# Performance work log

Hardware: AMD Instinct MI355X
Metric: run time of the kernel (lower is better)

The kernel has to match this reference:

```python
import jax, jax.numpy as jnp
import numpy as np

GLM_HIDDEN = 256
POS_EMB_DIM = 64
LN_EPS = 1e-5


def _pair_indices(seq_len, K):
    # emo index i (row), cau index j (col); keep |j-i| <= K (static mask)
    i = np.repeat(np.arange(seq_len), seq_len)
    j = np.tile(np.arange(seq_len), seq_len)
    rel = j - i
    keep = np.abs(rel) <= K
    return i[keep], j[keep], rel[keep]


def setup_inputs() -> dict:
    key = jax.random.key(0)
    ks = jax.random.split(key, 8)
    B, S, D, P, K = 32, 128, GLM_HIDDEN, POS_EMB_DIM, 8
    doc_sents_h = jax.random.normal(ks[0], (B, S, D), dtype=jnp.float32)
    pos_emb = jax.random.normal(ks[1], (2 * K + 1, P), dtype=jnp.float32) * 0.1
    in_dim = 2 * D + P
    W1 = jax.random.normal(ks[2], (D, in_dim), dtype=jnp.float32) * (1.0 / np.sqrt(in_dim))
    b1 = jnp.zeros((D,), dtype=jnp.float32)
    ln_g = jnp.ones((D,), dtype=jnp.float32)
    ln_b = jnp.zeros((D,), dtype=jnp.float32)
    W2 = jax.random.normal(ks[3], (1, D), dtype=jnp.float32) * (1.0 / np.sqrt(D))
    b2 = jnp.zeros((1,), dtype=jnp.float32)
    return {"doc_sents_h": doc_sents_h, "pos_emb": pos_emb, "W1": W1, "b1": b1,
            "ln_g": ln_g, "ln_b": ln_b, "W2": W2, "b2": b2, "K": K}


def reference(doc_sents_h, pos_emb, W1, b1, ln_g, ln_b, W2, b2, K):
    B, S, D = doc_sents_h.shape
    ii, jj, rel = _pair_indices(S, K)          # static numpy, shape [n_couple]
    # couples = [H_i ; H_j] for in-window pairs (replaces broadcast-concat + masked_select)
    couples = jnp.concatenate([doc_sents_h[:, ii], doc_sents_h[:, jj]], axis=-1)  # [B,n,2D]
    rel_idx = jnp.asarray(rel + K, dtype=jnp.int32)
    rpe = pos_emb[rel_idx]                     # [n, P]
    rf = jnp.asarray(rel, dtype=jnp.float32)
    kernel = jnp.exp(-jnp.square(rf[:, None] - rf[None, :]))  # [n, n]
    rpe = kernel @ rpe                         # [n, P] (same for every batch elem)
    pair = jnp.concatenate(
        [couples, jnp.broadcast_to(rpe[None], (B,) + rpe.shape)], axis=-1)  # [B,n,2D+P]
    h = jnp.einsum('bnf,df->bnd', pair, W1) + b1
    mu = jnp.mean(h, axis=-1, keepdims=True)
    var = jnp.mean(jnp.square(h - mu), axis=-1, keepdims=True)
    h = (h - mu) * jax.lax.rsqrt(var + LN_EPS) * ln_g + ln_b
    h = jax.nn.elu(h)                          # dropout is identity in eval
    scores = (jnp.einsum('bnd,od->bno', h, W2) + b2)[..., 0]  # [B, n]
    emo_cau_pos = jnp.stack([jnp.asarray(ii + 1), jnp.asarray(jj + 1)], axis=1)  # [n, 2]
    return scores, emo_cau_pos
```

## Files before the change

kernel.cpp:

```cpp
#include <hip/hip_runtime.h>
#include <math.h>

constexpr int kB = 32;
constexpr int kS = 128;
constexpr int kD = 256;
constexpr int kK = 8;
constexpr int kNPair = 2104;
constexpr int kInDim = 2 * kD + 64;
constexpr int kRows = kB * kS;

typedef __attribute__((ext_vector_type(8))) short short8;
typedef __attribute__((ext_vector_type(4))) float f32x4;

__device__ inline ushort f2b(float f) {
  union { float f; uint u; } v; v.f = f;
  uint r = v.u + 0x7FFF + ((v.u >> 16) & 1);
  return (ushort)(r >> 16);
}

__global__ __launch_bounds__(256) void gemm_uv_r(
    const float* __restrict__ H, const float* __restrict__ W1,
    const float* __restrict__ pos_emb, const float* __restrict__ b1,
    float* __restrict__ U, float* __restrict__ V, float* __restrict__ R) {
  __shared__ ushort As[64 * 256];
  __shared__ ushort Bs[64 * 256];
  const int tid = threadIdx.x;

  if (blockIdx.x == 512) {
    float* pe = (float*)As;
    for (int idx = tid; idx < 17 * 64; idx += 256) pe[idx] = pos_emb[idx];
    __syncthreads();
    const int d = tid;
    float w[64];
    const float* wr = W1 + d * kInDim + 2 * kD;
#pragma unroll
    for (int q = 0; q < 16; ++q) {
      float4 t4 = *(const float4*)(wr + q * 4);
      w[q * 4 + 0] = t4.x; w[q * 4 + 1] = t4.y;
      w[q * 4 + 2] = t4.z; w[q * 4 + 3] = t4.w;
    }
    float acc[17];
#pragma unroll
    for (int t = 0; t < 17; ++t) acc[t] = 0.f;
    for (int u = 0; u < 17; ++u) {
      float m = 0.f;
#pragma unroll
      for (int p = 0; p < 64; ++p) m += pe[u * 64 + p] * w[p];
      int au = u - kK; if (au < 0) au = -au;
      m *= (float)(kS - au);
#pragma unroll
      for (int t = 0; t < 17; ++t) {
        int dd = t - u;
        acc[t] += expf((float)(-(dd * dd))) * m;
      }
    }
#pragma unroll
    for (int t = 0; t < 17; ++t) R[t * kD + d] = acc[t] + b1[d];
    return;
  }

  const int mt = blockIdx.x & 63;
  const int nt = blockIdx.x >> 6;
  const int m0 = mt * 64;
  const int side = (nt >= 4) ? kD : 0;
  const int wbase = (nt & 3) * 64;

#pragma unroll
  for (int l = 0; l < 16; ++l) {
    int c = tid + l * 256;
    int row = c >> 6;
    int kq = (c & 63) << 2;
    int sw = (row << 8) + (kq ^ ((row & 7) << 3));
    float4 a4 = *(const float4*)(H + (m0 + row) * kD + kq);
    ushort4 au; au.x = f2b(a4.x); au.y = f2b(a4.y); au.z = f2b(a4.z); au.w = f2b(a4.w);
    *(ushort4*)(As + sw) = au;
    float4 b4 = *(const float4*)(W1 + (wbase + row) * kInDim + side + kq);
    ushort4 bu; bu.x = f2b(b4.x); bu.y = f2b(b4.y); bu.z = f2b(b4.z); bu.w = f2b(b4.w);
    *(ushort4*)(Bs + sw) = bu;
  }
  __syncthreads();

  const int lane = tid & 63;
  const int w = tid >> 6;
  const int wm = (w & 1) * 32;
  const int wn = (w >> 1) * 32;
  const int lr = lane & 15;
  const int lk = (lane >> 4) * 8;

  f32x4 acc[2][2] = {{{0.f,0.f,0.f,0.f},{0.f,0.f,0.f,0.f}},
                     {{0.f,0.f,0.f,0.f},{0.f,0.f,0.f,0.f}}};
#pragma unroll
  for (int kk = 0; kk < 8; ++kk) {
    const int k0 = kk * 32 + lk;
    short8 a[2], b[2];
#pragma unroll
    for (int mf = 0; mf < 2; ++mf) {
      int ra = wm + mf * 16 + lr;
      a[mf] = *(const short8*)(const void*)(As + (ra << 8) + (k0 ^ ((ra & 7) << 3)));
      int rb = wn + mf * 16 + lr;
      b[mf] = *(const short8*)(const void*)(Bs + (rb << 8) + (k0 ^ ((rb & 7) << 3)));
    }
#pragma unroll
    for (int mf = 0; mf < 2; ++mf)
#pragma unroll
      for (int nf = 0; nf < 2; ++nf)
        acc[mf][nf] = __builtin_amdgcn_mfma_f32_16x16x32_bf16(a[mf], b[nf], acc[mf][nf], 0, 0, 0);
  }

  const int rowg0 = m0 + wm + (lane >> 4) * 4;
  const int colg0 = nt * 64 + wn + lr;
#pragma unroll
  for (int mf = 0; mf < 2; ++mf)
#pragma unroll
    for (int nf = 0; nf < 2; ++nf) {
      int colg = colg0 + nf * 16;
      float* dst = (colg < kD) ? (U + colg) : (V + (colg - kD));
#pragma unroll
      for (int r = 0; r < 4; ++r) {
        int rowg = rowg0 + mf * 16 + r;
        dst[rowg * kD] = acc[mf][nf][r];
      }
    }
}

__global__ __launch_bounds__(256) void pair_score2(
    const float* __restrict__ U, const float* __restrict__ V,
    const float* __restrict__ R,
    const float* __restrict__ ln_g, const float* __restrict__ ln_b,
    const float* __restrict__ W2, const float* __restrict__ b2,
    float* __restrict__ out) {
  const int tid = threadIdx.x;
  const int l16 = tid & 15;
  const int grp = (blockIdx.x * 256 + tid) >> 4;
  const int t = grp % 17;
  const int bi = grp / 17;
  const int i = bi & (kS - 1);
  const int b = bi >> 7;
  const int j = i - kK + t;
  const bool valid = (j >= 0) && (j < kS);
  const int jc = valid ? j : 0;

  int start_i;
  if (i <= 8)        start_i = (i * i + 17 * i) / 2;
  else if (i <= 120) start_i = 100 + (i - 8) * 17;
  else { int m = i - 120; start_i = 2004 + 16 * m - (m * (m - 1)) / 2; }
  const int lower = (i - kK > 0) ? (i - kK) : 0;
  const int p = start_i + (j - lower);

  const float* Urow = U + (b * kS + i) * kD;
  const float* Vrow = V + (b * kS + jc) * kD;
  const float* Rrow = R + t * kD;

  float h[16];
  float s = 0.f, qs = 0.f;
#pragma unroll
  for (int q = 0; q < 4; ++q) {
    const int d = q * 64 + l16 * 4;
    float4 u4 = *(const float4*)(Urow + d);
    float4 v4 = *(const float4*)(Vrow + d);
    float4 r4 = *(const float4*)(Rrow + d);
    float h0 = u4.x + v4.x + r4.x;
    float h1 = u4.y + v4.y + r4.y;
    float h2 = u4.z + v4.z + r4.z;
    float h3 = u4.w + v4.w + r4.w;
    h[q * 4 + 0] = h0; h[q * 4 + 1] = h1; h[q * 4 + 2] = h2; h[q * 4 + 3] = h3;
    s += h0 + h1 + h2 + h3;
    qs += h0 * h0 + h1 * h1 + h2 * h2 + h3 * h3;
  }
#pragma unroll
  for (int off = 8; off > 0; off >>= 1) {
    s  += __shfl_xor(s, off);
    qs += __shfl_xor(qs, off);
  }
  const float mu = s * (1.0f / kD);
  const float var = qs * (1.0f / kD) - mu * mu;
  const float rs = rsqrtf(var + 1e-5f);

  float dot = 0.f;
#pragma unroll
  for (int q = 0; q < 4; ++q) {
    const int d = q * 64 + l16 * 4;
    float4 g4  = *(const float4*)(ln_g + d);
    float4 be4 = *(const float4*)(ln_b + d);
    float4 w4  = *(const float4*)(W2 + d);
    float y0 = (h[q * 4 + 0] - mu) * rs * g4.x + be4.x;
    float y1 = (h[q * 4 + 1] - mu) * rs * g4.y + be4.y;
    float y2 = (h[q * 4 + 2] - mu) * rs * g4.z + be4.z;
    float y3 = (h[q * 4 + 3] - mu) * rs * g4.w + be4.w;
    y0 = y0 > 0.f ? y0 : (__expf(y0) - 1.0f);
    y1 = y1 > 0.f ? y1 : (__expf(y1) - 1.0f);
    y2 = y2 > 0.f ? y2 : (__expf(y2) - 1.0f);
    y3 = y3 > 0.f ? y3 : (__expf(y3) - 1.0f);
    dot += y0 * w4.x + y1 * w4.y + y2 * w4.z + y3 * w4.w;
  }
#pragma unroll
  for (int off = 8; off > 0; off >>= 1) dot += __shfl_xor(dot, off);

  if (l16 == 0 && valid) {
    out[b * kNPair + p] = dot + b2[0];
    if (b == 0) {
      float* posout = out + kB * kNPair;
      posout[p * 2 + 0] = (float)(i + 1);
      posout[p * 2 + 1] = (float)(j + 1);
    }
  }
}

extern "C" void kernel_launch(void* const* d_in, const int* in_sizes, int n_in,
                              void* d_out, int out_size, void* d_ws, size_t ws_size,
                              hipStream_t stream) {
  const float* H       = (const float*)d_in[0];
  const float* pos_emb = (const float*)d_in[1];
  const float* W1      = (const float*)d_in[2];
  const float* b1      = (const float*)d_in[3];
  const float* ln_g    = (const float*)d_in[4];
  const float* ln_b    = (const float*)d_in[5];
  const float* W2      = (const float*)d_in[6];
  const float* b2      = (const float*)d_in[7];
  float* out = (float*)d_out;

  float* U = (float*)d_ws;
  float* V = U + kRows * kD;
  float* R = V + kRows * kD;

  gemm_uv_r<<<513, 256, 0, stream>>>(H, W1, pos_emb, b1, U, V, R);
  const int n_groups = kB * kS * 17;
  pair_score2<<<n_groups / 16, 256, 0, stream>>>(U, V, R, ln_g, ln_b, W2, b2, out);
}
```

Measured before the change: 42.66 us.

## Fuse projection GEMM, positional term and pair scoring into one kernel

Result: faster. 39.95 us (-6.3%).

```diff
diff --git a/kernel.cpp b/kernel.cpp
--- a/kernel.cpp
+++ b/kernel.cpp
@@ -6,8 +6,8 @@
 constexpr int kD = 256;
 constexpr int kK = 8;
 constexpr int kNPair = 2104;
-constexpr int kInDim = 2 * kD + 64;
-constexpr int kRows = kB * kS;
+constexpr int kInDim = 576;
+constexpr int kRS = 264;
 
 typedef __attribute__((ext_vector_type(8))) short short8;
 typedef __attribute__((ext_vector_type(4))) float f32x4;
@@ -18,190 +18,216 @@
   return (ushort)(r >> 16);
 }
 
-__global__ __launch_bounds__(256) void gemm_uv_r(
-    const float* __restrict__ H, const float* __restrict__ W1,
-    const float* __restrict__ pos_emb, const float* __restrict__ b1,
-    float* __restrict__ U, float* __restrict__ V, float* __restrict__ R) {
-  __shared__ ushort As[64 * 256];
-  __shared__ ushort Bs[64 * 256];
-  const int tid = threadIdx.x;
-
-  if (blockIdx.x == 512) {
-    float* pe = (float*)As;
-    for (int idx = tid; idx < 17 * 64; idx += 256) pe[idx] = pos_emb[idx];
-    __syncthreads();
-    const int d = tid;
-    float w[64];
-    const float* wr = W1 + d * kInDim + 2 * kD;
-#pragma unroll
-    for (int q = 0; q < 16; ++q) {
-      float4 t4 = *(const float4*)(wr + q * 4);
-      w[q * 4 + 0] = t4.x; w[q * 4 + 1] = t4.y;
-      w[q * 4 + 2] = t4.z; w[q * 4 + 3] = t4.w;
-    }
-    float acc[17];
-#pragma unroll
-    for (int t = 0; t < 17; ++t) acc[t] = 0.f;
-    for (int u = 0; u < 17; ++u) {
-      float m = 0.f;
-#pragma unroll
-      for (int p = 0; p < 64; ++p) m += pe[u * 64 + p] * w[p];
-      int au = u - kK; if (au < 0) au = -au;
-      m *= (float)(kS - au);
-#pragma unroll
-      for (int t = 0; t < 17; ++t) {
-        int dd = t - u;
-        acc[t] += expf((float)(-(dd * dd))) * m;
-      }
-    }
-#pragma unroll
-    for (int t = 0; t < 17; ++t) R[t * kD + d] = acc[t] + b1[d];
-    return;
-  }
-
-  const int mt = blockIdx.x & 63;
-  const int nt = blockIdx.x >> 6;
-  const int m0 = mt * 64;
-  const int side = (nt >= 4) ? kD : 0;
-  const int wbase = (nt & 3) * 64;
-
-#pragma unroll
-  for (int l = 0; l < 16; ++l) {
-    int c = tid + l * 256;
-    int row = c >> 6;
-    int kq = (c & 63) << 2;
-    int sw = (row << 8) + (kq ^ ((row & 7) << 3));
-    float4 a4 = *(const float4*)(H + (m0 + row) * kD + kq);
-    ushort4 au; au.x = f2b(a4.x); au.y = f2b(a4.y); au.z = f2b(a4.z); au.w = f2b(a4.w);
-    *(ushort4*)(As + sw) = au;
-    float4 b4 = *(const float4*)(W1 + (wbase + row) * kInDim + side + kq);
-    ushort4 bu; bu.x = f2b(b4.x); bu.y = f2b(b4.y); bu.z = f2b(b4.z); bu.w = f2b(b4.w);
-    *(ushort4*)(Bs + sw) = bu;
-  }
-  __syncthreads();
-
-  const int lane = tid & 63;
-  const int w = tid >> 6;
-  const int wm = (w & 1) * 32;
-  const int wn = (w >> 1) * 32;
-  const int lr = lane & 15;
-  const int lk = (lane >> 4) * 8;
-
-  f32x4 acc[2][2] = {{{0.f,0.f,0.f,0.f},{0.f,0.f,0.f,0.f}},
-                     {{0.f,0.f,0.f,0.f},{0.f,0.f,0.f,0.f}}};
-#pragma unroll
-  for (int kk = 0; kk < 8; ++kk) {
-    const int k0 = kk * 32 + lk;
-    short8 a[2], b[2];
-#pragma unroll
-    for (int mf = 0; mf < 2; ++mf) {
-      int ra = wm + mf * 16 + lr;
-      a[mf] = *(const short8*)(const void*)(As + (ra << 8) + (k0 ^ ((ra & 7) << 3)));
-      int rb = wn + mf * 16 + lr;
-      b[mf] = *(const short8*)(const void*)(Bs + (rb << 8) + (k0 ^ ((rb & 7) << 3)));
-    }
-#pragma unroll
-    for (int mf = 0; mf < 2; ++mf)
-#pragma unroll
-      for (int nf = 0; nf < 2; ++nf)
-        acc[mf][nf] = __builtin_amdgcn_mfma_f32_16x16x32_bf16(a[mf], b[nf], acc[mf][nf], 0, 0, 0);
-  }
-
-  const int rowg0 = m0 + wm + (lane >> 4) * 4;
-  const int colg0 = nt * 64 + wn + lr;
-#pragma unroll
-  for (int mf = 0; mf < 2; ++mf)
-#pragma unroll
-    for (int nf = 0; nf < 2; ++nf) {
-      int colg = colg0 + nf * 16;
-      float* dst = (colg < kD) ? (U + colg) : (V + (colg - kD));
-#pragma unroll
-      for (int r = 0; r < 4; ++r) {
-        int rowg = rowg0 + mf * 16 + r;
-        dst[rowg * kD] = acc[mf][nf][r];
-      }
-    }
-}
-
-__global__ __launch_bounds__(256) void pair_score2(
-    const float* __restrict__ U, const float* __restrict__ V,
-    const float* __restrict__ R,
+__global__ __launch_bounds__(256, 1) void fused_all(
+    const float* __restrict__ H, const float* __restrict__ pos_emb,
+    const float* __restrict__ W1, const float* __restrict__ b1,
     const float* __restrict__ ln_g, const float* __restrict__ ln_b,
     const float* __restrict__ W2, const float* __restrict__ b2,
     float* __restrict__ out) {
+  __shared__ __align__(16) ushort sH[48 * 256];
+  __shared__ __align__(16) ushort sW[64 * 256];
+  __shared__ __align__(16) ushort sKpe[32 * 64];
+  __shared__ float sU[16 * kRS];
+  __shared__ float sV[48 * kRS];
+  __shared__ float sR[17 * kRS];
+  __shared__ float sG[256], sBe[256], sWo[256], sB1[256];
+  __shared__ float sB2v;
+
   const int tid = threadIdx.x;
-  const int l16 = tid & 15;
-  const int grp = (blockIdx.x * 256 + tid) >> 4;
-  const int t = grp % 17;
-  const int bi = grp / 17;
-  const int i = bi & (kS - 1);
-  const int b = bi >> 7;
-  const int j = i - kK + t;
-  const bool valid = (j >= 0) && (j < kS);
-  const int jc = valid ? j : 0;
-
-  int start_i;
-  if (i <= 8)        start_i = (i * i + 17 * i) / 2;
-  else if (i <= 120) start_i = 100 + (i - 8) * 17;
-  else { int m = i - 120; start_i = 2004 + 16 * m - (m * (m - 1)) / 2; }
-  const int lower = (i - kK > 0) ? (i - kK) : 0;
-  const int p = start_i + (j - lower);
-
-  const float* Urow = U + (b * kS + i) * kD;
-  const float* Vrow = V + (b * kS + jc) * kD;
-  const float* Rrow = R + t * kD;
-
-  float h[16];
-  float s = 0.f, qs = 0.f;
+  const int b = blockIdx.x >> 3;
+  const int i0 = (blockIdx.x & 7) << 4;
+  int ws_ = i0 - 16; if (ws_ < 0) ws_ = 0; if (ws_ > 80) ws_ = 80;
+  const int ws = ws_;
+  const int oi = i0 - ws;
+
+  sG[tid] = ln_g[tid]; sBe[tid] = ln_b[tid]; sWo[tid] = W2[tid]; sB1[tid] = b1[tid];
+  if (tid == 0) sB2v = b2[0];
+
+#pragma unroll
+  for (int l = 0; l < 12; ++l) {
+    int c = tid + l * 256, row = c >> 6, kq = (c & 63) << 2;
+    float4 a4 = *(const float4*)(H + (b * kS + ws + row) * kD + kq);
+    ushort4 u; u.x = f2b(a4.x); u.y = f2b(a4.y); u.z = f2b(a4.z); u.w = f2b(a4.w);
+    *(ushort4*)&sH[row * 256 + (kq ^ ((row & 7) << 3))] = u;
+  }
+#pragma unroll
+  for (int l = 0; l < 16; ++l) {
+    int c = tid + l * 256, d = c >> 4, kq = (c & 15) << 2;
+    float4 a4 = *(const float4*)(W1 + d * kInDim + 512 + kq);
+    ushort4 u; u.x = f2b(a4.x); u.y = f2b(a4.y); u.z = f2b(a4.z); u.w = f2b(a4.w);
+    *(ushort4*)&sW[d * 64 + (kq ^ ((d & 7) << 3))] = u;
+  }
+  {
+    const int pg = (tid & 15) << 2;
+#pragma unroll
+    for (int pass = 0; pass < 2; ++pass) {
+      int t = (tid >> 4) + pass * 16;
+      float a0 = 0.f, a1 = 0.f, a2 = 0.f, a3 = 0.f;
+      if (t < 17) {
+        for (int u = 0; u < 17; ++u) {
+          int du = t - u, au = u - kK; if (au < 0) au = -au;
+          float wt = __expf((float)(-(du * du))) * (float)(kS - au);
+          float4 pe = *(const float4*)(pos_emb + u * 64 + pg);
+          a0 += wt * pe.x; a1 += wt * pe.y; a2 += wt * pe.z; a3 += wt * pe.w;
+        }
+      }
+      ushort4 u; u.x = f2b(a0); u.y = f2b(a1); u.z = f2b(a2); u.w = f2b(a3);
+      *(ushort4*)&sKpe[t * 64 + (pg ^ ((t & 7) << 3))] = u;
+    }
+  }
+  __syncthreads();
+
+  const int lane = tid & 63;
+  const int w = tid >> 6;
+  const int lr = lane & 15;
+  const int lk = (lane >> 4) << 3;
+  const int swz = (lr & 7) << 3;
+  const int r0 = (lane >> 4) << 2;
+
+  {
+    f32x4 racc[2][4] = {{{0,0,0,0},{0,0,0,0},{0,0,0,0},{0,0,0,0}},
+                        {{0,0,0,0},{0,0,0,0},{0,0,0,0},{0,0,0,0}}};
+#pragma unroll
+    for (int kk = 0; kk < 2; ++kk) {
+      int k0 = (kk << 5) + lk;
+      short8 a0 = *(const short8*)(const void*)&sKpe[lr * 64 + (k0 ^ swz)];
+      short8 a1 = *(const short8*)(const void*)&sKpe[(16 + lr) * 64 + (k0 ^ swz)];
+#pragma unroll
+      for (int n = 0; n < 4; ++n) {
+        int drow = ((w << 2) + n) * 16 + lr;
+        short8 bf = *(const short8*)(const void*)&sW[drow * 64 + (k0 ^ swz)];
+        racc[0][n] = __builtin_amdgcn_mfma_f32_16x16x32_bf16(a0, bf, racc[0][n], 0, 0, 0);
+        racc[1][n] = __builtin_amdgcn_mfma_f32_16x16x32_bf16(a1, bf, racc[1][n], 0, 0, 0);
+      }
+    }
+#pragma unroll
+    for (int m = 0; m < 2; ++m)
+#pragma unroll
+      for (int r = 0; r < 4; ++r) {
+        int t = m * 16 + r0 + r;
+        if (t < 17) {
+#pragma unroll
+          for (int n = 0; n < 4; ++n) {
+            int d = ((w << 2) + n) * 16 + lr;
+            sR[t * kRS + d] = racc[m][n][r] + sB1[d];
+          }
+        }
+      }
+  }
+  __syncthreads();
+
+  for (int nt = 0; nt < 8; ++nt) {
+#pragma unroll
+    for (int l = 0; l < 16; ++l) {
+      int c = tid + l * 256, row = c >> 6, kq = (c & 63) << 2;
+      int cg = (nt << 6) + row;
+      const float* src = W1 + (cg & 255) * kInDim + ((cg < 256) ? 0 : 256) + kq;
+      float4 a4 = *(const float4*)src;
+      ushort4 u; u.x = f2b(a4.x); u.y = f2b(a4.y); u.z = f2b(a4.z); u.w = f2b(a4.w);
+      *(ushort4*)&sW[row * 256 + (kq ^ ((row & 7) << 3))] = u;
+    }
+    __syncthreads();
+    f32x4 acc[3] = {{0,0,0,0},{0,0,0,0},{0,0,0,0}};
+    const int brow = (w << 4) + lr;
+#pragma unroll
+    for (int kk = 0; kk < 8; ++kk) {
+      int k0 = (kk << 5) + lk;
+      short8 bf = *(const short8*)(const void*)&sW[brow * 256 + (k0 ^ swz)];
+#pragma unroll
+      for (int m = 0; m < 3; ++m) {
+        short8 af = *(const short8*)(const void*)&sH[(m * 16 + lr) * 256 + (k0 ^ swz)];
+        acc[m] = __builtin_amdgcn_mfma_f32_16x16x32_bf16(af, bf, acc[m], 0, 0, 0);
+      }
+    }
+    const int cg = (nt << 6) + (w << 4) + lr;
+#pragma unroll
+    for (int m = 0; m < 3; ++m)
+#pragma unroll
+      for (int r = 0; r < 4; ++r) {
+        int rw = m * 16 + r0 + r;
+        float val = acc[m][r];
+        if (cg < 256) {
+          unsigned ur = (unsigned)(rw - oi);
+          if (ur < 16u) sU[ur * kRS + cg] = val;
+        } else {
+          sV[rw * kRS + (cg - 256)] = val;
+        }
+      }
+    __syncthreads();
+  }
+
+  const int g = tid >> 4, l16 = tid & 15;
+  float4 Gp[4], Bp[4], Wp[4];
 #pragma unroll
   for (int q = 0; q < 4; ++q) {
-    const int d = q * 64 + l16 * 4;
-    float4 u4 = *(const float4*)(Urow + d);
-    float4 v4 = *(const float4*)(Vrow + d);
-    float4 r4 = *(const float4*)(Rrow + d);
-    float h0 = u4.x + v4.x + r4.x;
-    float h1 = u4.y + v4.y + r4.y;
-    float h2 = u4.z + v4.z + r4.z;
-    float h3 = u4.w + v4.w + r4.w;
-    h[q * 4 + 0] = h0; h[q * 4 + 1] = h1; h[q * 4 + 2] = h2; h[q * 4 + 3] = h3;
-    s += h0 + h1 + h2 + h3;
-    qs += h0 * h0 + h1 * h1 + h2 * h2 + h3 * h3;
-  }
-#pragma unroll
-  for (int off = 8; off > 0; off >>= 1) {
-    s  += __shfl_xor(s, off);
-    qs += __shfl_xor(qs, off);
-  }
-  const float mu = s * (1.0f / kD);
-  const float var = qs * (1.0f / kD) - mu * mu;
-  const float rs = rsqrtf(var + 1e-5f);
-
-  float dot = 0.f;
-#pragma unroll
-  for (int q = 0; q < 4; ++q) {
-    const int d = q * 64 + l16 * 4;
-    float4 g4  = *(const float4*)(ln_g + d);
-    float4 be4 = *(const float4*)(ln_b + d);
-    float4 w4  = *(const float4*)(W2 + d);
-    float y0 = (h[q * 4 + 0] - mu) * rs * g4.x + be4.x;
-    float y1 = (h[q * 4 + 1] - mu) * rs * g4.y + be4.y;
-    float y2 = (h[q * 4 + 2] - mu) * rs * g4.z + be4.z;
-    float y3 = (h[q * 4 + 3] - mu) * rs * g4.w + be4.w;
-    y0 = y0 > 0.f ? y0 : (__expf(y0) - 1.0f);
-    y1 = y1 > 0.f ? y1 : (__expf(y1) - 1.0f);
-    y2 = y2 > 0.f ? y2 : (__expf(y2) - 1.0f);
-    y3 = y3 > 0.f ? y3 : (__expf(y3) - 1.0f);
-    dot += y0 * w4.x + y1 * w4.y + y2 * w4.z + y3 * w4.w;
-  }
-#pragma unroll
-  for (int off = 8; off > 0; off >>= 1) dot += __shfl_xor(dot, off);
-
-  if (l16 == 0 && valid) {
-    out[b * kNPair + p] = dot + b2[0];
-    if (b == 0) {
-      float* posout = out + kB * kNPair;
-      posout[p * 2 + 0] = (float)(i + 1);
-      posout[p * 2 + 1] = (float)(j + 1);
+    int d = (q << 6) + (l16 << 2);
+    Gp[q] = *(const float4*)&sG[d];
+    Bp[q] = *(const float4*)&sBe[d];
+    Wp[q] = *(const float4*)&sWo[d];
+  }
+  const float bias2 = sB2v;
+
+  for (int s = g; s < 272; s += 16) {
+    int ir = s / 17, t = s - ir * 17;
+    int i = i0 + ir, j = i - kK + t;
+    if (j < 0 || j >= kS) continue;
+    int vr = j - ws;
+    int start_i;
+    if (i <= 8)        start_i = (i * i + 17 * i) / 2;
+    else if (i <= 120) start_i = 100 + (i - 8) * 17;
+    else { int m = i - 120; start_i = 2004 + 16 * m - (m * (m - 1)) / 2; }
+    const int lower = (i - kK > 0) ? (i - kK) : 0;
+    const int p = start_i + (j - lower);
+
+    const float* Ur = &sU[ir * kRS];
+    const float* Vr = &sV[vr * kRS];
+    const float* Rr = &sR[t * kRS];
+    float h[16]; float ssum = 0.f, qsum = 0.f;
+#pragma unroll
+    for (int q = 0; q < 4; ++q) {
+      int d = (q << 6) + (l16 << 2);
+      float4 u4 = *(const float4*)(Ur + d);
+      float4 v4 = *(const float4*)(Vr + d);
+      float4 r4 = *(const float4*)(Rr + d);
+      float h0 = u4.x + v4.x + r4.x;
+      float h1 = u4.y + v4.y + r4.y;
+      float h2 = u4.z + v4.z + r4.z;
+      float h3 = u4.w + v4.w + r4.w;
+      h[q * 4 + 0] = h0; h[q * 4 + 1] = h1; h[q * 4 + 2] = h2; h[q * 4 + 3] = h3;
+      ssum += h0 + h1 + h2 + h3;
+      qsum += h0 * h0 + h1 * h1 + h2 * h2 + h3 * h3;
+    }
+#pragma unroll
+    for (int off = 8; off > 0; off >>= 1) {
+      ssum += __shfl_xor(ssum, off);
+      qsum += __shfl_xor(qsum, off);
+    }
+    const float mu = ssum * (1.0f / kD);
+    const float var = qsum * (1.0f / kD) - mu * mu;
+    const float rs = rsqrtf(var + 1e-5f);
+    float dot = 0.f;
+#pragma unroll
+    for (int q = 0; q < 4; ++q) {
+      float y0 = (h[q * 4 + 0] - mu) * rs * Gp[q].x + Bp[q].x;
+      float y1 = (h[q * 4 + 1] - mu) * rs * Gp[q].y + Bp[q].y;
+      float y2 = (h[q * 4 + 2] - mu) * rs * Gp[q].z + Bp[q].z;
+      float y3 = (h[q * 4 + 3] - mu) * rs * Gp[q].w + Bp[q].w;
+      y0 = y0 > 0.f ? y0 : (__expf(y0) - 1.0f);
+      y1 = y1 > 0.f ? y1 : (__expf(y1) - 1.0f);
+      y2 = y2 > 0.f ? y2 : (__expf(y2) - 1.0f);
+      y3 = y3 > 0.f ? y3 : (__expf(y3) - 1.0f);
+      dot += y0 * Wp[q].x + y1 * Wp[q].y + y2 * Wp[q].z + y3 * Wp[q].w;
+    }
+#pragma unroll
+    for (int off = 8; off > 0; off >>= 1) dot += __shfl_xor(dot, off);
+
+    if (l16 == 0) {
+      out[b * kNPair + p] = dot + bias2;
+      if (b == 0) {
+        float* po = out + kB * kNPair;
+        po[2 * p + 0] = (float)(i + 1);
+        po[2 * p + 1] = (float)(j + 1);
+      }
     }
   }
 }
@@ -209,6 +235,7 @@
 extern "C" void kernel_launch(void* const* d_in, const int* in_sizes, int n_in,
                               void* d_out, int out_size, void* d_ws, size_t ws_size,
                               hipStream_t stream) {
+  (void)in_sizes; (void)n_in; (void)d_ws; (void)ws_size; (void)out_size;
   const float* H       = (const float*)d_in[0];
   const float* pos_emb = (const float*)d_in[1];
   const float* W1      = (const float*)d_in[2];
@@ -219,11 +246,5 @@
   const float* b2      = (const float*)d_in[7];
   float* out = (float*)d_out;
 
-  float* U = (float*)d_ws;
-  float* V = U + kRows * kD;
-  float* R = V + kRows * kD;
-
-  gemm_uv_r<<<513, 256, 0, stream>>>(H, W1, pos_emb, b1, U, V, R);
-  const int n_groups = kB * kS * 17;
-  pair_score2<<<n_groups / 16, 256, 0, stream>>>(U, V, R, ln_g, ln_b, W2, b2, out);
+  fused_all<<<kB * 8, 256, 0, stream>>>(H, pos_emb, W1, b1, ln_g, ln_b, W2, b2, out);
 }
```

## Split bf16 conversion into prep kernel and use LDS-free per-wave GEMM tiles

Applied to the files above, without the earlier changes.

After: 58.21 us. +36.5%, slower.

```diff
diff --git a/kernel.cpp b/kernel.cpp
--- a/kernel.cpp
+++ b/kernel.cpp
@@ -6,8 +6,8 @@
 constexpr int kD = 256;
 constexpr int kK = 8;
 constexpr int kNPair = 2104;
-constexpr int kInDim = 2 * kD + 64;
-constexpr int kRows = kB * kS;
+constexpr int kInDim = 576;
+constexpr int kRows = 4096;
 
 typedef __attribute__((ext_vector_type(8))) short short8;
 typedef __attribute__((ext_vector_type(4))) float f32x4;
@@ -18,21 +18,38 @@
   return (ushort)(r >> 16);
 }
 
-__global__ __launch_bounds__(256) void gemm_uv_r(
-    const float* __restrict__ H, const float* __restrict__ W1,
-    const float* __restrict__ pos_emb, const float* __restrict__ b1,
-    float* __restrict__ U, float* __restrict__ V, float* __restrict__ R) {
-  __shared__ ushort As[64 * 256];
-  __shared__ ushort Bs[64 * 256];
-  const int tid = threadIdx.x;
-
-  if (blockIdx.x == 512) {
-    float* pe = (float*)As;
+__global__ __launch_bounds__(256) void prep(
+    const float* __restrict__ H, const float* __restrict__ pos_emb,
+    const float* __restrict__ W1, const float* __restrict__ b1,
+    ushort* __restrict__ Hb, ushort* __restrict__ Wb, float* __restrict__ Rg) {
+  const int blk = blockIdx.x, tid = threadIdx.x;
+  if (blk < 256) {
+#pragma unroll
+    for (int l = 0; l < 4; ++l) {
+      int c = blk * 1024 + l * 256 + tid;
+      float4 a = *(const float4*)(H + c * 4);
+      ushort4 u; u.x = f2b(a.x); u.y = f2b(a.y); u.z = f2b(a.z); u.w = f2b(a.w);
+      *(ushort4*)(Hb + c * 4) = u;
+    }
+  } else if (blk < 288) {
+    int bb = blk - 256;
+#pragma unroll
+    for (int l = 0; l < 4; ++l) {
+      int c = bb * 1024 + l * 256 + tid;
+      int r = c >> 6;
+      int kq = (c & 63) << 2;
+      const float* src = W1 + (r & 255) * kInDim + ((r < 256) ? 0 : 256) + kq;
+      float4 a = *(const float4*)src;
+      ushort4 u; u.x = f2b(a.x); u.y = f2b(a.y); u.z = f2b(a.z); u.w = f2b(a.w);
+      *(ushort4*)(Wb + r * 256 + kq) = u;
+    }
+  } else {
+    __shared__ float pe[17 * 64];
     for (int idx = tid; idx < 17 * 64; idx += 256) pe[idx] = pos_emb[idx];
     __syncthreads();
     const int d = tid;
     float w[64];
-    const float* wr = W1 + d * kInDim + 2 * kD;
+    const float* wr = W1 + d * kInDim + 512;
 #pragma unroll
     for (int q = 0; q < 16; ++q) {
       float4 t4 = *(const float4*)(wr + q * 4);
@@ -55,72 +72,40 @@
       }
     }
 #pragma unroll
-    for (int t = 0; t < 17; ++t) R[t * kD + d] = acc[t] + b1[d];
-    return;
-  }
-
-  const int mt = blockIdx.x & 63;
-  const int nt = blockIdx.x >> 6;
-  const int m0 = mt * 64;
-  const int side = (nt >= 4) ? kD : 0;
-  const int wbase = (nt & 3) * 64;
-
-#pragma unroll
-  for (int l = 0; l < 16; ++l) {
-    int c = tid + l * 256;
-    int row = c >> 6;
-    int kq = (c & 63) << 2;
-    int sw = (row << 8) + (kq ^ ((row & 7) << 3));
-    float4 a4 = *(const float4*)(H + (m0 + row) * kD + kq);
-    ushort4 au; au.x = f2b(a4.x); au.y = f2b(a4.y); au.z = f2b(a4.z); au.w = f2b(a4.w);
-    *(ushort4*)(As + sw) = au;
-    float4 b4 = *(const float4*)(W1 + (wbase + row) * kInDim + side + kq);
-    ushort4 bu; bu.x = f2b(b4.x); bu.y = f2b(b4.y); bu.z = f2b(b4.z); bu.w = f2b(b4.w);
-    *(ushort4*)(Bs + sw) = bu;
-  }
-  __syncthreads();
-
+    for (int t = 0; t < 17; ++t) Rg[t * kD + d] = acc[t] + b1[d];
+  }
+}
+
+__global__ __launch_bounds__(256) void gemm_tiles(
+    const ushort* __restrict__ Hb, const ushort* __restrict__ Wb,
+    float* __restrict__ U, float* __restrict__ V) {
+  const int tid = threadIdx.x;
   const int lane = tid & 63;
-  const int w = tid >> 6;
-  const int wm = (w & 1) * 32;
-  const int wn = (w >> 1) * 32;
+  const int gw = blockIdx.x * 4 + (tid >> 6);
+  const int m = gw & 255;
+  const int n = gw >> 8;
   const int lr = lane & 15;
-  const int lk = (lane >> 4) * 8;
-
-  f32x4 acc[2][2] = {{{0.f,0.f,0.f,0.f},{0.f,0.f,0.f,0.f}},
-                     {{0.f,0.f,0.f,0.f},{0.f,0.f,0.f,0.f}}};
+  const int lk = (lane >> 4) << 3;
+  const ushort* Arow = Hb + (m * 16 + lr) * 256 + lk;
+  const ushort* Brow = Wb + (n * 16 + lr) * 256 + lk;
+  short8 a[8], bb[8];
 #pragma unroll
   for (int kk = 0; kk < 8; ++kk) {
-    const int k0 = kk * 32 + lk;
-    short8 a[2], b[2];
-#pragma unroll
-    for (int mf = 0; mf < 2; ++mf) {
-      int ra = wm + mf * 16 + lr;
-      a[mf] = *(const short8*)(const void*)(As + (ra << 8) + (k0 ^ ((ra & 7) << 3)));
-      int rb = wn + mf * 16 + lr;
-      b[mf] = *(const short8*)(const void*)(Bs + (rb << 8) + (k0 ^ ((rb & 7) << 3)));
-    }
-#pragma unroll
-    for (int mf = 0; mf < 2; ++mf)
-#pragma unroll
-      for (int nf = 0; nf < 2; ++nf)
-        acc[mf][nf] = __builtin_amdgcn_mfma_f32_16x16x32_bf16(a[mf], b[nf], acc[mf][nf], 0, 0, 0);
-  }
-
-  const int rowg0 = m0 + wm + (lane >> 4) * 4;
-  const int colg0 = nt * 64 + wn + lr;
-#pragma unroll
-  for (int mf = 0; mf < 2; ++mf)
-#pragma unroll
-    for (int nf = 0; nf < 2; ++nf) {
-      int colg = colg0 + nf * 16;
-      float* dst = (colg < kD) ? (U + colg) : (V + (colg - kD));
-#pragma unroll
-      for (int r = 0; r < 4; ++r) {
-        int rowg = rowg0 + mf * 16 + r;
-        dst[rowg * kD] = acc[mf][nf][r];
-      }
-    }
+    a[kk]  = *(const short8*)(const void*)(Arow + kk * 32);
+    bb[kk] = *(const short8*)(const void*)(Brow + kk * 32);
+  }
+  f32x4 acc0 = {0.f, 0.f, 0.f, 0.f}, acc1 = {0.f, 0.f, 0.f, 0.f};
+#pragma unroll
+  for (int kk = 0; kk < 8; kk += 2) {
+    acc0 = __builtin_amdgcn_mfma_f32_16x16x32_bf16(a[kk],     bb[kk],     acc0, 0, 0, 0);
+    acc1 = __builtin_amdgcn_mfma_f32_16x16x32_bf16(a[kk + 1], bb[kk + 1], acc1, 0, 0, 0);
+  }
+  const int cg = n * 16 + lr;
+  float* dst = (cg < kD) ? (U + cg) : (V + (cg - kD));
+  const int rowbase = m * 16 + ((lane >> 4) << 2);
+#pragma unroll
+  for (int r = 0; r < 4; ++r)
+    dst[(rowbase + r) * kD] = acc0[r] + acc1[r];
 }
 
 __global__ __launch_bounds__(256) void pair_score2(
@@ -209,6 +194,7 @@
 extern "C" void kernel_launch(void* const* d_in, const int* in_sizes, int n_in,
                               void* d_out, int out_size, void* d_ws, size_t ws_size,
                               hipStream_t stream) {
+  (void)in_sizes; (void)n_in; (void)ws_size; (void)out_size;
   const float* H       = (const float*)d_in[0];
   const float* pos_emb = (const float*)d_in[1];
   const float* W1      = (const float*)d_in[2];
@@ -219,11 +205,14 @@
   const float* b2      = (const float*)d_in[7];
   float* out = (float*)d_out;
 
-  float* U = (float*)d_ws;
-  float* V = U + kRows * kD;
-  float* R = V + kRows * kD;
-
-  gemm_uv_r<<<513, 256, 0, stream>>>(H, W1, pos_emb, b1, U, V, R);
+  ushort* Hb = (ushort*)d_ws;
+  ushort* Wb = Hb + kRows * kD;
+  float*  Rg = (float*)(Wb + 512 * kD);
+  float*  U  = Rg + 17 * kD;
+  float*  V  = U + kRows * kD;
+
+  prep<<<289, 256, 0, stream>>>(H, pos_emb, W1, b1, Hb, Wb, Rg);
+  gemm_tiles<<<2048, 256, 0, stream>>>(Hb, Wb, U, V);
   const int n_groups = kB * kS * 17;
-  pair_score2<<<n_groups / 16, 256, 0, stream>>>(U, V, R, ln_g, ln_b, W2, b2, out);
-}
+  pair_score2<<<n_groups / 16, 256, 0, stream>>>(U, V, Rg, ln_g, ln_b, W2, b2, out);
+}
```
